# Optimization experiments

Measured on AMD Instinct MI355X. Metric: run time of the kernel, lower is better.

The kernel has to match this reference:

```python
import jax, jax.numpy as jnp
import numpy as np

N = 2048       # num nodes
IN = 512       # in_features == hidden_features == out_features (residuals)
HID = 512
OUT = 512
H = 8          # num_heads
DX = 256       # x feature dim
LN_EPS = 1e-5
NORM_EPS = 1e-12


def _layernorm(x, g, b):
    mu = jnp.mean(x, axis=-1, keepdims=True)
    var = jnp.mean(jnp.square(x - mu), axis=-1, keepdims=True)
    return (x - mu) * jax.lax.rsqrt(var + LN_EPS) * g + b


def _l1_normalize(x):
    # torch F.normalize(p=1): x / max(||x||_1, eps)
    n = jnp.sum(jnp.abs(x), axis=-1, keepdims=True)
    return x / jnp.maximum(n, NORM_EPS)


def _linear_init(key, out_f, in_f):
    kw, kb = jax.random.split(key)
    bound = 1.0 / np.sqrt(in_f)
    W = jax.random.uniform(kw, (out_f, in_f), jnp.float32, -bound, bound)
    b = jax.random.uniform(kb, (out_f,), jnp.float32, -bound, bound)
    return W, b


def setup_inputs() -> dict:
    key = jax.random.key(0)
    ks = jax.random.split(key, 10)
    h = jax.random.normal(ks[0], (N, IN), jnp.float32)
    x = jax.random.uniform(ks[1], (N, DX), jnp.float32)
    Wk, bk = _linear_init(ks[2], HID, IN)
    Wq, bq = _linear_init(ks[3], HID, IN)
    Wv, bv = _linear_init(ks[4], HID, IN)
    Wm1, bm1 = _linear_init(ks[5], H, H + 1)   # mixing_x2h
    Wm2, bm2 = _linear_init(ks[6], 1, H)
    Wfc, bfc = _linear_init(ks[7], OUT, HID + 4)
    ln_g = jnp.ones((IN,), jnp.float32)
    ln_b = jnp.zeros((IN,), jnp.float32)
    lnf_g = jnp.ones((HID,), jnp.float32)
    lnf_b = jnp.zeros((HID,), jnp.float32)
    return dict(h=h, x=x, ln_g=ln_g, ln_b=ln_b, Wk=Wk, bk=bk, Wq=Wq, bq=bq,
                Wv=Wv, bv=bv, Wm1=Wm1, bm1=bm1, Wm2=Wm2, bm2=bm2,
                lnf_g=lnf_g, lnf_b=lnf_b, Wfc=Wfc, bfc=bfc)


def reference(h, x, ln_g, ln_b, Wk, bk, Wq, bq, Wv, bv, Wm1, bm1, Wm2, bm2,
              lnf_g, lnf_b, Wfc, bfc):
    h0, x0 = h, x
    hn = _layernorm(h, ln_g, ln_b)
    xn = _l1_normalize(x)

    k = (hn @ Wk.T + bk).reshape(N, HID // H, H)
    q = (hn @ Wq.T + bq).reshape(N, HID // H, H)
    a_h = jnp.einsum('xyb,zyb->xzb', k, q)          # [N, N, H]
    a_x = xn @ xn.T                                  # [N, N]

    # head mixing: Linear(H+1 -> H) over concat([a_x, a_h])
    a_cat = jnp.concatenate([a_x[..., None], a_h], axis=-1)  # [N, N, H+1]
    a_h = a_cat @ Wm1.T + bm1                                # [N, N, H]
    a_x = (a_h @ Wm2.T + bm2)[..., 0] + a_x                  # [N, N]

    a_h = jax.nn.softmax(a_h, axis=-1)               # softmax over heads
    a_x = _l1_normalize(a_x)

    # per-row stats of a_x -> [N, 4]
    i = jnp.concatenate([
        jnp.diagonal(a_x)[:, None],
        jnp.sum(a_x, axis=-1, keepdims=True),
        jnp.std(a_x, axis=-1, ddof=1, keepdims=True),
        jnp.max(a_x, axis=-1, keepdims=True),
    ], axis=-1)

    v = (hn @ Wv.T + bv).reshape(N, OUT // H, H)
    hm = jnp.einsum('xyb,yzb->xzb', a_h, v).reshape(N, HID)
    xm = a_x @ xn

    hm = hm + h0
    xm = xm + x0
    _h0 = hm

    hf = _layernorm(hm, lnf_g, lnf_b)
    hf = jnp.concatenate([hf, i], axis=-1)           # [N, HID+4]
    hf = jax.nn.elu(hf @ Wfc.T + bfc)
    hf = hf + _h0
    return (hf, xm)
```

## Files before the change

### kernel.cpp

```cpp
#include <hip/hip_runtime.h>
#include <math.h>

#define NN 2048
#define FD 512
#define DXF 256
#define JC 8
#define CHKJ (NN/JC)
#define ITI 32
#define JTW 64
#define NIT (CHKJ/JTW)
#define KC (NN/4)

typedef unsigned short u16;
typedef unsigned int u32;
typedef __attribute__((ext_vector_type(8))) short s16x8;
typedef __attribute__((ext_vector_type(4))) float f32x4;

__device__ __forceinline__ f32x4 MFMA16(s16x8 a, s16x8 b, f32x4 c) {
  return __builtin_amdgcn_mfma_f32_16x16x32_bf16(a, b, c, 0, 0, 0);
}
__device__ __forceinline__ float blo(u32 u) { return __uint_as_float(u << 16); }
__device__ __forceinline__ float bhi(u32 u) { return __uint_as_float(u & 0xffff0000u); }
__device__ __forceinline__ float b2f(u16 v) { return __uint_as_float((u32)v << 16); }
__device__ __forceinline__ u16 bf1(float f) {
  u32 u = __float_as_uint(f);
  u += 0x7fffu + ((u >> 16) & 1u);
  return (u16)(u >> 16);
}
__device__ __forceinline__ u32 pkbf(float a, float b) {
  u32 ua = __float_as_uint(a), ub = __float_as_uint(b);
  ua += 0x7fffu + ((ua >> 16) & 1u);
  ub += 0x7fffu + ((ub >> 16) & 1u);
  return (ua >> 16) | (ub & 0xffff0000u);
}

__global__ void preproc_k(
    const float* __restrict__ h, const float* __restrict__ ln_g,
    const float* __restrict__ ln_b, u16* __restrict__ hnB,
    const float* __restrict__ x, u16* __restrict__ xnB,
    const float* __restrict__ Wk, const float* __restrict__ Wq,
    const float* __restrict__ Wv, u16* __restrict__ wkB, u16* __restrict__ wqB,
    u16* __restrict__ wvB, const float* __restrict__ Wfc, u16* __restrict__ wfcB) {
  int bid = blockIdx.x, t = threadIdx.x;
  __shared__ float red[4][2];
  if (bid < NN) {
    int r = bid;
    float2 v = ((const float2*)(h + (size_t)r * FD))[t];
    float2 w = make_float2(v.x + v.y, v.x * v.x + v.y * v.y);
#pragma unroll
    for (int o = 32; o > 0; o >>= 1) { w.x += __shfl_xor(w.x, o); w.y += __shfl_xor(w.y, o); }
    if ((t & 63) == 0) { red[t >> 6][0] = w.x; red[t >> 6][1] = w.y; }
    __syncthreads();
    float S  = (red[0][0] + red[1][0]) + (red[2][0] + red[3][0]);
    float SQ = (red[0][1] + red[1][1]) + (red[2][1] + red[3][1]);
    float mean = S * (1.f / FD);
    float var  = SQ * (1.f / FD) - mean * mean;
    float rs = rsqrtf(var + 1e-5f);
    float2 gg = ((const float2*)ln_g)[t], bb = ((const float2*)ln_b)[t];
    float ox = (v.x - mean) * rs * gg.x + bb.x;
    float oy = (v.y - mean) * rs * gg.y + bb.y;
    *(u32*)(hnB + (size_t)r * FD + 2 * t) = pkbf(ox, oy);
  } else if (bid < 2 * NN) {
    int r = bid - NN;
    float v = x[(size_t)r * DXF + t];
    float s = fabsf(v);
#pragma unroll
    for (int o = 32; o > 0; o >>= 1) s += __shfl_xor(s, o);
    if ((t & 63) == 0) red[t >> 6][0] = s;
    __syncthreads();
    float S = (red[0][0] + red[1][0]) + (red[2][0] + red[3][0]);
    float inv = 1.f / fmaxf(S, 1e-12f);
    xnB[(size_t)r * DXF + t] = bf1(v * inv);
  } else if (bid < 2 * NN + 1536) {
    int idx = bid - 2 * NN;
    int z = idx >> 9;
    int i = ((idx & 511) << 8) + t;
    const float* W = (z == 0) ? Wk : (z == 1) ? Wq : Wv;
    u16* O = (z == 0) ? wkB : (z == 1) ? wqB : wvB;
    float2 v = ((const float2*)W)[i];
    ((u32*)O)[i] = pkbf(v.x, v.y);
  } else {
    int i = (bid - (2 * NN + 1536)) * 256 + t;
    if (i < 512 * 272) {
      int r = i / 272, c2 = (i - r * 272) * 2;
      float a = (c2 < 516) ? Wfc[r * 516 + c2] : 0.f;
      float b = (c2 + 1 < 516) ? Wfc[r * 516 + c2 + 1] : 0.f;
      ((u32*)wfcB)[i] = pkbf(a, b);
    }
  }
}

__global__ void xnt_k(const u16* __restrict__ xnB, u16* __restrict__ xnTg) {
  __shared__ u16 tile[16][264];
  int t = threadIdx.x;
  int r0 = blockIdx.x * 16;
#pragma unroll
  for (int s = 0; s < 2; ++s) {
    int c = s * 256 + t;
    int db = c & 31, row = c >> 5;
    *(uint4*)&tile[row][db * 8] = *(const uint4*)(xnB + (size_t)(r0 + row) * DXF + db * 8);
  }
  __syncthreads();
#pragma unroll
  for (int s = 0; s < 2; ++s) {
    int c = s * 256 + t;
    int jb = c & 1, d = c >> 1;
    u32 p[4];
#pragma unroll
    for (int e2 = 0; e2 < 4; ++e2) {
      u16 a = tile[jb * 8 + e2 * 2][d], b = tile[jb * 8 + e2 * 2 + 1][d];
      p[e2] = (u32)a | ((u32)b << 16);
    }
    *(uint4*)(xnTg + (size_t)d * NN + r0 + jb * 8) = make_uint4(p[0], p[1], p[2], p[3]);
  }
}

__global__ __launch_bounds__(256) void proj3_k(
    const u16* __restrict__ A,
    const u16* __restrict__ W0, const u16* __restrict__ W1, const u16* __restrict__ W2,
    const float* __restrict__ b0, const float* __restrict__ b1, const float* __restrict__ b2,
    u16* __restrict__ kP, u16* __restrict__ qP, u16* __restrict__ vPT) {
  int z = blockIdx.z;
  const u16* B = (z == 0) ? W0 : (z == 1) ? W1 : W2;
  const float* bias = (z == 0) ? b0 : (z == 1) ? b1 : b2;
  int t = threadIdx.x, w = t >> 6, lane = t & 63, g = lane >> 4, li = lane & 15;
  int m0 = blockIdx.x * 64 + (w & 1) * 32;
  int n0 = blockIdx.y * 64 + (w >> 1) * 32;
  f32x4 acc[2][2] = {};
  for (int k0 = 0; k0 < FD; k0 += 32) {
    s16x8 a0 = *(const s16x8*)(A + (size_t)(m0 + li) * FD + k0 + g * 8);
    s16x8 a1 = *(const s16x8*)(A + (size_t)(m0 + 16 + li) * FD + k0 + g * 8);
    s16x8 bA = *(const s16x8*)(B + (size_t)(n0 + li) * FD + k0 + g * 8);
    s16x8 bB = *(const s16x8*)(B + (size_t)(n0 + 16 + li) * FD + k0 + g * 8);
    acc[0][0] = MFMA16(a0, bA, acc[0][0]);
    acc[0][1] = MFMA16(a0, bB, acc[0][1]);
    acc[1][0] = MFMA16(a1, bA, acc[1][0]);
    acc[1][1] = MFMA16(a1, bB, acc[1][1]);
  }
#pragma unroll
  for (int ms = 0; ms < 2; ++ms)
#pragma unroll
    for (int ns = 0; ns < 2; ++ns) {
      int ncol = n0 + ns * 16 + li;
      float bv = bias[ncol];
      if (z < 2) {
        u16* out = z ? qP : kP;
#pragma unroll
        for (int r = 0; r < 4; ++r) {
          int i = m0 + ms * 16 + g * 4 + r;
          out[((size_t)(ncol & 7) * NN + i) * 64 + (ncol >> 3)] = bf1(acc[ms][ns][r] + bv);
        }
      } else {
        u16 e[4];
#pragma unroll
        for (int r = 0; r < 4; ++r) e[r] = bf1(acc[ms][ns][r] + bv);
        u32 p0 = (u32)e[0] | ((u32)e[1] << 16);
        u32 p1 = (u32)e[2] | ((u32)e[3] << 16);
        int ib = m0 + ms * 16 + g * 4;
        *(uint2*)(vPT + ((size_t)((ncol & 7) * 64 + (ncol >> 3))) * NN + ib) =
            make_uint2(p0, p1);
      }
    }
}

__global__ __launch_bounds__(256) void fc_gemm_k(
    const u16* __restrict__ A, const u16* __restrict__ B,
    const float* __restrict__ bias, const float* __restrict__ res,
    float* __restrict__ C) {
  int t = threadIdx.x, w = t >> 6, lane = t & 63, g = lane >> 4, li = lane & 15;
  int m0 = blockIdx.x * 32 + (w & 1) * 16;
  int n0 = blockIdx.y * 32 + (w >> 1) * 16;
  f32x4 acc = {};
  for (int k0 = 0; k0 < 544; k0 += 32) {
    s16x8 a0 = *(const s16x8*)(A + (size_t)(m0 + li) * 544 + k0 + g * 8);
    s16x8 b0 = *(const s16x8*)(B + (size_t)(n0 + li) * 544 + k0 + g * 8);
    acc = MFMA16(a0, b0, acc);
  }
  int ncol = n0 + li;
  float bv = bias[ncol];
#pragma unroll
  for (int r = 0; r < 4; ++r) {
    int i = m0 + g * 4 + r;
    float cv = acc[r] + bv;
    cv = (cv > 0.f) ? cv : (expf(cv) - 1.f);
    cv += res[(size_t)i * FD + ncol];
    C[(size_t)i * FD + ncol] = cv;
  }
}

__global__ __launch_bounds__(256) void xm_split_k(
    const u16* __restrict__ axg, const u16* __restrict__ xnTg,
    float* __restrict__ xmp, float* __restrict__ stq) {
  int t = threadIdx.x, w = t >> 6, lane = t & 63, g = lane >> 4, li = lane & 15;
  int m0 = blockIdx.x * 64 + (w & 1) * 32;
  int n0 = blockIdx.y * 64 + (w >> 1) * 32;
  int z = blockIdx.z;
  const int kb = z * KC;
  f32x4 acc[2][2] = {};
  float sab[2] = {0.f, 0.f}, ssu[2] = {0.f, 0.f}, ssq[2] = {0.f, 0.f};
  float smx[2] = {-1e30f, -1e30f};
  const bool do_stats = (blockIdx.y == 0) && ((w >> 1) == 0);
  for (int k0 = 0; k0 < KC; k0 += 32) {
    s16x8 a0 = *(const s16x8*)(axg + (size_t)(m0 + li) * NN + kb + k0 + g * 8);
    s16x8 a1 = *(const s16x8*)(axg + (size_t)(m0 + 16 + li) * NN + kb + k0 + g * 8);
    s16x8 bA = *(const s16x8*)(xnTg + (size_t)(n0 + li) * NN + kb + k0 + g * 8);
    s16x8 bB = *(const s16x8*)(xnTg + (size_t)(n0 + 16 + li) * NN + kb + k0 + g * 8);
    acc[0][0] = MFMA16(a0, bA, acc[0][0]);
    acc[0][1] = MFMA16(a0, bB, acc[0][1]);
    acc[1][0] = MFMA16(a1, bA, acc[1][0]);
    acc[1][1] = MFMA16(a1, bB, acc[1][1]);
    if (do_stats) {
#pragma unroll
      for (int ms = 0; ms < 2; ++ms) {
        u32 pu[4];
        *(s16x8*)pu = ms ? a1 : a0;
#pragma unroll
        for (int q2 = 0; q2 < 4; ++q2) {
          float x0 = blo(pu[q2]), x1 = bhi(pu[q2]);
          sab[ms] += fabsf(x0) + fabsf(x1);
          ssu[ms] += x0 + x1;
          ssq[ms] += x0 * x0 + x1 * x1;
          smx[ms] = fmaxf(smx[ms], fmaxf(x0, x1));
        }
      }
    }
  }
  if (do_stats) {
#pragma unroll
    for (int off = 16; off < 64; off <<= 1) {
#pragma unroll
      for (int ms = 0; ms < 2; ++ms) {
        sab[ms] += __shfl_xor(sab[ms], off);
        ssu[ms] += __shfl_xor(ssu[ms], off);
        ssq[ms] += __shfl_xor(ssq[ms], off);
        smx[ms] = fmaxf(smx[ms], __shfl_xor(smx[ms], off));
      }
    }
    if (g == 0) {
#pragma unroll
      for (int ms = 0; ms < 2; ++ms) {
        size_t base = ((size_t)z * NN + m0 + ms * 16 + li) * 4;
        stq[base + 0] = sab[ms]; stq[base + 1] = ssu[ms];
        stq[base + 2] = ssq[ms]; stq[base + 3] = smx[ms];
      }
    }
  }
#pragma unroll
  for (int ms = 0; ms < 2; ++ms)
#pragma unroll
    for (int ns = 0; ns < 2; ++ns) {
      int ncol = n0 + ns * 16 + li;
#pragma unroll
      for (int r = 0; r < 4; ++r) {
        int i = m0 + ms * 16 + g * 4 + r;
        xmp[(size_t)z * NN * DXF + (size_t)i * DXF + ncol] = acc[ms][ns][r];
      }
    }
}

__global__ __launch_bounds__(512, 2) void fused_mfma_k(
    const u16* __restrict__ kP, const u16* __restrict__ qP,
    const u16* __restrict__ vPT, const u16* __restrict__ xnB,
    const float* __restrict__ Wm1, const float* __restrict__ bm1,
    const float* __restrict__ Wm2, const float* __restrict__ bm2,
    u16* __restrict__ hmPart, u16* __restrict__ axg, float* __restrict__ stPd) {
  __shared__ __align__(16) unsigned char L[81920];
  const int O_KI = 0, O_XNI = 32768, O_P = 49152;
  const int t = threadIdx.x, w = t >> 6, lane = t & 63;
  const int g = lane >> 4, li = lane & 15;
  const int i0 = blockIdx.x * ITI, chunk = blockIdx.y;
  const int si = w & 1;
  const int jL = (w >> 1) * 16 + li;
  const int iRow = si * 16 + li;
  const int prow = si * 16 + li;

  float W1[8][9], B1v[8], w2v[8];
#pragma unroll
  for (int o = 0; o < 8; ++o) {
    B1v[o] = bm1[o];
    w2v[o] = Wm2[o];
#pragma unroll
    for (int b3 = 0; b3 < 9; ++b3) W1[o][b3] = Wm1[o * 9 + b3];
  }
  const float b2v = bm2[0];

#pragma unroll
  for (int s = 0; s < 4; ++s) {
    int c = s * 512 + t;
    int yb = c & 7, il = (c >> 3) & 31, b = c >> 8;
    uint4 v = *(const uint4*)(kP + ((size_t)b * NN + i0 + il) * 64 + yb * 8);
    *(uint4*)(L + O_KI + b * 4096 + il * 128 + ((yb ^ (il & 7)) << 4)) = v;
  }
#pragma unroll
  for (int s = 0; s < 2; ++s) {
    int c = s * 512 + t;
    int db = c & 31, il = c >> 5;
    uint4 v = *(const uint4*)(xnB + (size_t)(i0 + il) * DXF + db * 8);
    *(uint4*)(L + O_XNI + il * 512 + ((db ^ (il & 7)) << 4)) = v;
  }
  __syncthreads();

  f32x4 hmA[2][4];
#pragma unroll
  for (int a = 0; a < 2; ++a)
#pragma unroll
    for (int c = 0; c < 4; ++c) hmA[a][c] = (f32x4)(0.f);

  for (int it = 0; it < NIT; ++it) {
    const int j0 = chunk * CHKJ + it * JTW;
    f32x4 accS[9];
#pragma unroll
    for (int a = 0; a < 9; ++a) accS[a] = (f32x4)(0.f);
#pragma unroll
    for (int b = 0; b < 8; ++b)
#pragma unroll
      for (int ks = 0; ks < 2; ++ks) {
        int blk = ks * 4 + g;
        s16x8 af = *(const s16x8*)(L + O_KI + b * 4096 + iRow * 128 +
                                   ((blk ^ (iRow & 7)) << 4));
        s16x8 bf = *(const s16x8*)(qP + ((size_t)b * NN + j0 + jL) * 64 + ks * 32 + g * 8);
        accS[b] = MFMA16(af, bf, accS[b]);
      }
#pragma unroll
    for (int ks = 0; ks < 8; ++ks) {
      int blk = ks * 4 + g;
      s16x8 af = *(const s16x8*)(L + O_XNI + iRow * 512 + ((blk ^ (iRow & 7)) << 4));
      s16x8 bf = *(const s16x8*)(xnB + (size_t)(j0 + jL) * DXF + ks * 32 + g * 8);
      accS[8] = MFMA16(af, bf, accS[8]);
    }
    s16x8 vf0[2][4];
#pragma unroll
    for (int kb = 0; kb < 2; ++kb)
#pragma unroll
      for (int zt = 0; zt < 4; ++zt)
        vf0[kb][zt] = *(const s16x8*)(vPT + ((size_t)((w >> 1) * 2 + 0) * 64 + zt * 16 + li) * NN +
                                      j0 + kb * 32 + g * 8);
    __syncthreads();
#pragma unroll
    for (int r = 0; r < 4; ++r) {
      float sb[8];
#pragma unroll
      for (int b = 0; b < 8; ++b) sb[b] = accS[b][r];
      float ax = accS[8][r];
      float m[8];
#pragma unroll
      for (int o = 0; o < 8; ++o) {
        float a = B1v[o] + W1[o][0] * ax;
#pragma unroll
        for (int b = 0; b < 8; ++b) a += W1[o][1 + b] * sb[b];
        m[o] = a;
      }
      float axn = b2v + ax;
#pragma unroll
      for (int o = 0; o < 8; ++o) axn += w2v[o] * m[o];
      const int iL2 = si * 16 + g * 4 + r;
      const int iG = i0 + iL2, jG = j0 + jL;
      axg[(size_t)iG * NN + jG] = bf1(axn);
      if (iG == jG) stPd[iG] = axn;
      float mx = m[0];
#pragma unroll
      for (int o = 1; o < 8; ++o) mx = fmaxf(mx, m[o]);
      float es[8], esum = 0.f;
#pragma unroll
      for (int o = 0; o < 8; ++o) { es[o] = __expf(m[o] - mx); esum += es[o]; }
      float inv = 1.f / esum;
      const int base = iL2 * 128 + (((jL >> 3) ^ (iL2 & 7)) << 4) + (jL & 7) * 2;
#pragma unroll
      for (int b = 0; b < 8; ++b)
        *(u16*)(L + O_P + b * 4096 + base) = bf1(es[b] * inv);
    }
    s16x8 vf1[2][4];
#pragma unroll
    for (int kb = 0; kb < 2; ++kb)
#pragma unroll
      for (int zt = 0; zt < 4; ++zt)
        vf1[kb][zt] = *(const s16x8*)(vPT + ((size_t)((w >> 1) * 2 + 1) * 64 + zt * 16 + li) * NN +
                                      j0 + kb * 32 + g * 8);
    __syncthreads();
#pragma unroll
    for (int hh = 0; hh < 2; ++hh) {
      const int hd = (w >> 1) * 2 + hh;
#pragma unroll
      for (int kb = 0; kb < 2; ++kb) {
        s16x8 pa = *(const s16x8*)(L + O_P + hd * 4096 + prow * 128 +
                                   (((kb * 4 + g) ^ (prow & 7)) << 4));
#pragma unroll
        for (int zt = 0; zt < 4; ++zt) {
          s16x8 vf = hh ? vf1[kb][zt] : vf0[kb][zt];
          hmA[hh][zt] = MFMA16(pa, vf, hmA[hh][zt]);
        }
      }
    }
  }
#pragma unroll
  for (int hh = 0; hh < 2; ++hh) {
    const int hd = (w >> 1) * 2 + hh;
#pragma unroll
    for (int zt = 0; zt < 4; ++zt)
#pragma unroll
      for (int r = 0; r < 4; ++r) {
        int i = i0 + si * 16 + g * 4 + r;
        int z = zt * 16 + li;
        hmPart[((size_t)(chunk * 8 + hd) * NN + i) * 64 + z] = bf1(hmA[hh][zt][r]);
      }
  }
}

__global__ void epilogue1_k(
    const float* __restrict__ h, const float* __restrict__ x,
    const u16* __restrict__ hmp, const float* __restrict__ xmp,
    const float* __restrict__ stq, const float* __restrict__ stPd,
    const float* __restrict__ lnf_g, const float* __restrict__ lnf_b,
    float* __restrict__ hmf, u16* __restrict__ hfeB, float* __restrict__ out_xm) {
  int r = blockIdx.x, t = threadIdx.x;
  int c0 = 2 * t, c1 = c0 + 1;
  float2 acc = ((const float2*)(h + (size_t)r * FD))[t];
#pragma unroll
  for (int ch = 0; ch < JC; ++ch) {
    acc.x += b2f(hmp[((size_t)(ch * 8 + (c0 & 7)) * NN + r) * 64 + (c0 >> 3)]);
    acc.y += b2f(hmp[((size_t)(ch * 8 + (c1 & 7)) * NN + r) * 64 + (c1 >> 3)]);
  }
  ((float2*)(hmf + (size_t)r * FD))[t] = acc;
  float2 w = make_float2(acc.x + acc.y, acc.x * acc.x + acc.y * acc.y);
#pragma unroll
  for (int o = 32; o > 0; o >>= 1) { w.x += __shfl_xor(w.x, o); w.y += __shfl_xor(w.y, o); }
  __shared__ float red[4][2];
  __shared__ float s_inv;
  if ((t & 63) == 0) { red[t >> 6][0] = w.x; red[t >> 6][1] = w.y; }
  __syncthreads();
  float S  = (red[0][0] + red[1][0]) + (red[2][0] + red[3][0]);
  float SQ = (red[0][1] + red[1][1]) + (red[2][1] + red[3][1]);
  float mean = S * (1.f / FD);
  float var  = SQ * (1.f / FD) - mean * mean;
  float rs = rsqrtf(var + 1e-5f);
  float2 g2 = ((const float2*)lnf_g)[t], b2 = ((const float2*)lnf_b)[t];
  float ox = (acc.x - mean) * rs * g2.x + b2.x;
  float oy = (acc.y - mean) * rs * g2.y + b2.y;
  *(u32*)(hfeB + (size_t)r * 544 + c0) = pkbf(ox, oy);
  if (t == 0) {
    float sab = 0.f, ssu = 0.f, ssq = 0.f, smx = -1e30f;
#pragma unroll
    for (int c = 0; c < 4; ++c) {
      size_t b = ((size_t)c * NN + r) * 4;
      sab += stq[b + 0]; ssu += stq[b + 1]; ssq += stq[b + 2];
      smx = fmaxf(smx, stq[b + 3]);
    }
    float diag = stPd[r];
    float L1 = fmaxf(sab, 1e-12f);
    float inv = 1.f / L1;
    float stdv = sqrtf(fmaxf((ssq - ssu * ssu * (1.f / 2048.f)) * (1.f / 2047.f), 0.f)) * inv;
    u16* he = hfeB + (size_t)r * 544;
    he[512] = bf1(diag * inv); he[513] = bf1(ssu * inv);
    he[514] = bf1(stdv);       he[515] = bf1(smx * inv);
    s_inv = inv;
  }
  if (t < 14) *(u32*)(hfeB + (size_t)r * 544 + 516 + 2 * t) = 0;
  __syncthreads();
  float inv = s_inv;
  float xv = xmp[(size_t)r * DXF + t] + xmp[(size_t)NN * DXF + (size_t)r * DXF + t] +
             xmp[2 * (size_t)NN * DXF + (size_t)r * DXF + t] +
             xmp[3 * (size_t)NN * DXF + (size_t)r * DXF + t];
  out_xm[(size_t)r * DXF + t] = xv * inv + x[(size_t)r * DXF + t];
}

extern "C" void kernel_launch(void* const* d_in, const int* in_sizes, int n_in,
                              void* d_out, int out_size, void* d_ws, size_t ws_size,
                              hipStream_t stream) {
  (void)in_sizes; (void)n_in; (void)out_size; (void)ws_size;
  const float* h    = (const float*)d_in[0];
  const float* x    = (const float*)d_in[1];
  const float* ln_g = (const float*)d_in[2];
  const float* ln_b = (const float*)d_in[3];
  const float* Wk   = (const float*)d_in[4];
  const float* bk   = (const float*)d_in[5];
  const float* Wq   = (const float*)d_in[6];
  const float* bq   = (const float*)d_in[7];
  const float* Wv   = (const float*)d_in[8];
  const float* bv   = (const float*)d_in[9];
  const float* Wm1  = (const float*)d_in[10];
  const float* bm1  = (const float*)d_in[11];
  const float* Wm2  = (const float*)d_in[12];
  const float* bm2  = (const float*)d_in[13];
  const float* lnf_g = (const float*)d_in[14];
  const float* lnf_b = (const float*)d_in[15];
  const float* Wfc  = (const float*)d_in[16];
  const float* bfc  = (const float*)d_in[17];

  char* wsb = (char*)d_ws;
  size_t off = 0;
  auto alloc = [&](size_t bytes) { char* p = wsb + off; off += (bytes + 255) & ~(size_t)255; return p; };
  u16*   hnB  = (u16*)alloc((size_t)NN * FD * 2);
  u16*   wkB  = (u16*)alloc((size_t)FD * FD * 2);
  u16*   wqB  = (u16*)alloc((size_t)FD * FD * 2);
  u16*   wvB  = (u16*)alloc((size_t)FD * FD * 2);
  u16*   wfcB = (u16*)alloc((size_t)512 * 544 * 2);
  u16*   kP   = (u16*)alloc((size_t)8 * NN * 64 * 2);
  u16*   qP   = (u16*)alloc((size_t)8 * NN * 64 * 2);
  u16*   vPT  = (u16*)alloc((size_t)8 * 64 * NN * 2);
  u16*   xnB  = (u16*)alloc((size_t)NN * DXF * 2);
  u16*   xnTg = (u16*)alloc((size_t)DXF * NN * 2);
  u16*   axg  = (u16*)alloc((size_t)NN * NN * 2);
  u16*   hmp  = (u16*)alloc((size_t)JC * 8 * NN * 64 * 2);
  float* xmp  = (float*)alloc((size_t)4 * NN * DXF * 4);
  float* stq  = (float*)alloc((size_t)4 * NN * 4 * 4);
  float* stPd = (float*)alloc((size_t)NN * 4);
  float* hmf  = (float*)alloc((size_t)NN * FD * 4);
  u16*   hfeB = (u16*)alloc((size_t)NN * 544 * 2);
  float* out_hf = (float*)d_out;
  float* out_xm = out_hf + (size_t)NN * FD;

  preproc_k<<<2 * NN + 1536 + 544, 256, 0, stream>>>(
      h, ln_g, ln_b, hnB, x, xnB, Wk, Wq, Wv, wkB, wqB, wvB, Wfc, wfcB);
  xnt_k<<<NN / 16, 256, 0, stream>>>(xnB, xnTg);

  proj3_k<<<dim3(32, 8, 3), 256, 0, stream>>>(hnB, wkB, wqB, wvB, bk, bq, bv, kP, qP, vPT);

  fused_mfma_k<<<dim3(NN / ITI, JC), 512, 0, stream>>>(kP, qP, vPT, xnB, Wm1, bm1, Wm2, bm2,
                                                       hmp, axg, stPd);

  xm_split_k<<<dim3(32, 4, 4), 256, 0, stream>>>(axg, xnTg, xmp, stq);

  epilogue1_k<<<NN, 256, 0, stream>>>(h, x, hmp, xmp, stq, stPd, lnf_g, lnf_b, hmf, hfeB, out_xm);

  fc_gemm_k<<<dim3(64, 16), 256, 0, stream>>>(hfeB, wfcB, bfc, hmf, out_hf);
}
```

Baseline: 159.7 us.

## Store q, v and xn in MFMA-fragment order for contiguous wave loads

The projection kernel now writes q and v, and the transpose kernel writes a copy of xn, pre-arranged in per-lane MFMA operand order. The fused attention kernel can then load each B fragment as one contiguous 1 KB block per wave instead of strided rows. This targets uncoalesced global loads in the main loop. In exchange the producer kernels use more complex scattered stores, and the extra xn copy adds some memory traffic.

New measurement: 141.7 us, median of 2. 11.3% less time.

```diff
diff --git a/kernel.cpp b/kernel.cpp
--- a/kernel.cpp
+++ b/kernel.cpp
@@ -90,7 +90,8 @@
   }
 }
 
-__global__ void xnt_k(const u16* __restrict__ xnB, u16* __restrict__ xnTg) {
+__global__ void xnt_k(const u16* __restrict__ xnB, u16* __restrict__ xnTg,
+                      u16* __restrict__ xnF) {
   __shared__ u16 tile[16][264];
   int t = threadIdx.x;
   int r0 = blockIdx.x * 16;
@@ -113,13 +114,21 @@
     }
     *(uint4*)(xnTg + (size_t)d * NN + r0 + jb * 8) = make_uint4(p[0], p[1], p[2], p[3]);
   }
+#pragma unroll
+  for (int s = 0; s < 2; ++s) {
+    int idx = s * 256 + t;
+    int ks = idx >> 6, lane = idx & 63;
+    int row = lane & 15, db = ks * 32 + (lane >> 4) * 8;
+    uint4 v = *(const uint4*)&tile[row][db];
+    *(uint4*)(xnF + (((size_t)(r0 >> 4) * 8 + ks) * 64 + lane) * 8) = v;
+  }
 }
 
 __global__ __launch_bounds__(256) void proj3_k(
     const u16* __restrict__ A,
     const u16* __restrict__ W0, const u16* __restrict__ W1, const u16* __restrict__ W2,
     const float* __restrict__ b0, const float* __restrict__ b1, const float* __restrict__ b2,
-    u16* __restrict__ kP, u16* __restrict__ qP, u16* __restrict__ vPT) {
+    u16* __restrict__ kP, u16* __restrict__ qF, u16* __restrict__ vF) {
   int z = blockIdx.z;
   const u16* B = (z == 0) ? W0 : (z == 1) ? W1 : W2;
   const float* bias = (z == 0) ? b0 : (z == 1) ? b1 : b2;
@@ -143,22 +152,33 @@
     for (int ns = 0; ns < 2; ++ns) {
       int ncol = n0 + ns * 16 + li;
       float bv = bias[ncol];
-      if (z < 2) {
-        u16* out = z ? qP : kP;
+      if (z == 0) {
 #pragma unroll
         for (int r = 0; r < 4; ++r) {
           int i = m0 + ms * 16 + g * 4 + r;
-          out[((size_t)(ncol & 7) * NN + i) * 64 + (ncol >> 3)] = bf1(acc[ms][ns][r] + bv);
+          kP[((size_t)(ncol & 7) * NN + i) * 64 + (ncol >> 3)] = bf1(acc[ms][ns][r] + bv);
+        }
+      } else if (z == 1) {
+#pragma unroll
+        for (int r = 0; r < 4; ++r) {
+          int i = m0 + ms * 16 + g * 4 + r;
+          size_t idx = ((size_t)(i >> 4) * 8 + (ncol & 7)) * 1024 +
+                       (size_t)(ncol >> 8) * 512 +
+                       (size_t)((i & 15) | (((ncol >> 6) & 3) << 4)) * 8 +
+                       ((ncol >> 3) & 7);
+          qF[idx] = bf1(acc[ms][ns][r] + bv);
         }
       } else {
-        u16 e[4];
-#pragma unroll
-        for (int r = 0; r < 4; ++r) e[r] = bf1(acc[ms][ns][r] + bv);
-        u32 p0 = (u32)e[0] | ((u32)e[1] << 16);
-        u32 p1 = (u32)e[2] | ((u32)e[3] << 16);
-        int ib = m0 + ms * 16 + g * 4;
-        *(uint2*)(vPT + ((size_t)((ncol & 7) * 64 + (ncol >> 3))) * NN + ib) =
-            make_uint2(p0, p1);
+        u16 e4[4];
+#pragma unroll
+        for (int r = 0; r < 4; ++r) e4[r] = bf1(acc[ms][ns][r] + bv);
+        u32 p0 = (u32)e4[0] | ((u32)e4[1] << 16);
+        u32 p1 = (u32)e4[2] | ((u32)e4[3] << 16);
+        int ibase = m0 + ms * 16 + g * 4;
+        int lane_w = ((ncol >> 3) & 15) | (((ibase >> 3) & 3) << 4);
+        size_t base = ((((size_t)(m0 >> 5) * 8 + (ncol & 7)) * 4 + (ncol >> 7)) * 64 + lane_w) * 8 +
+                      ((g & 1) * 4);
+        *(uint2*)(vF + base) = make_uint2(p0, p1);
       }
     }
 }
@@ -259,8 +279,9 @@
 }
 
 __global__ __launch_bounds__(512, 2) void fused_mfma_k(
-    const u16* __restrict__ kP, const u16* __restrict__ qP,
-    const u16* __restrict__ vPT, const u16* __restrict__ xnB,
+    const u16* __restrict__ kP, const u16* __restrict__ qF,
+    const u16* __restrict__ vF, const u16* __restrict__ xnB,
+    const u16* __restrict__ xnF,
     const float* __restrict__ Wm1, const float* __restrict__ bm1,
     const float* __restrict__ Wm2, const float* __restrict__ bm2,
     u16* __restrict__ hmPart, u16* __restrict__ axg, float* __restrict__ stPd) {
@@ -270,7 +291,8 @@
   const int g = lane >> 4, li = lane & 15;
   const int i0 = blockIdx.x * ITI, chunk = blockIdx.y;
   const int si = w & 1;
-  const int jL = (w >> 1) * 16 + li;
+  const int jw = w >> 1;
+  const int jL = jw * 16 + li;
   const int iRow = si * 16 + li;
   const int prow = si * 16 + li;
 
@@ -308,6 +330,8 @@
 
   for (int it = 0; it < NIT; ++it) {
     const int j0 = chunk * CHKJ + it * JTW;
+    const int jt = (j0 >> 4) + jw;
+    const int jb32 = j0 >> 5;
     f32x4 accS[9];
 #pragma unroll
     for (int a = 0; a < 9; ++a) accS[a] = (f32x4)(0.f);
@@ -318,14 +342,15 @@
         int blk = ks * 4 + g;
         s16x8 af = *(const s16x8*)(L + O_KI + b * 4096 + iRow * 128 +
                                    ((blk ^ (iRow & 7)) << 4));
-        s16x8 bf = *(const s16x8*)(qP + ((size_t)b * NN + j0 + jL) * 64 + ks * 32 + g * 8);
+        s16x8 bf = *(const s16x8*)(qF + (((size_t)jt * 8 + b) * 2 + ks) * 512 +
+                                   (size_t)lane * 8);
         accS[b] = MFMA16(af, bf, accS[b]);
       }
 #pragma unroll
     for (int ks = 0; ks < 8; ++ks) {
       int blk = ks * 4 + g;
       s16x8 af = *(const s16x8*)(L + O_XNI + iRow * 512 + ((blk ^ (iRow & 7)) << 4));
-      s16x8 bf = *(const s16x8*)(xnB + (size_t)(j0 + jL) * DXF + ks * 32 + g * 8);
+      s16x8 bf = *(const s16x8*)(xnF + ((size_t)jt * 8 + ks) * 512 + (size_t)lane * 8);
       accS[8] = MFMA16(af, bf, accS[8]);
     }
     s16x8 vf0[2][4];
@@ -333,8 +358,8 @@
     for (int kb = 0; kb < 2; ++kb)
 #pragma unroll
       for (int zt = 0; zt < 4; ++zt)
-        vf0[kb][zt] = *(const s16x8*)(vPT + ((size_t)((w >> 1) * 2 + 0) * 64 + zt * 16 + li) * NN +
-                                      j0 + kb * 32 + g * 8);
+        vf0[kb][zt] = *(const s16x8*)(vF + ((((size_t)(jb32 + kb) * 8 + jw * 2 + 0) * 4 + zt) * 512) +
+                                      (size_t)lane * 8);
     __syncthreads();
 #pragma unroll
     for (int r = 0; r < 4; ++r) {
@@ -374,12 +399,12 @@
     for (int kb = 0; kb < 2; ++kb)
 #pragma unroll
       for (int zt = 0; zt < 4; ++zt)
-        vf1[kb][zt] = *(const s16x8*)(vPT + ((size_t)((w >> 1) * 2 + 1) * 64 + zt * 16 + li) * NN +
-                                      j0 + kb * 32 + g * 8);
+        vf1[kb][zt] = *(const s16x8*)(vF + ((((size_t)(jb32 + kb) * 8 + jw * 2 + 1) * 4 + zt) * 512) +
+                                      (size_t)lane * 8);
     __syncthreads();
 #pragma unroll
     for (int hh = 0; hh < 2; ++hh) {
-      const int hd = (w >> 1) * 2 + hh;
+      const int hd = jw * 2 + hh;
 #pragma unroll
       for (int kb = 0; kb < 2; ++kb) {
         s16x8 pa = *(const s16x8*)(L + O_P + hd * 4096 + prow * 128 +
@@ -394,7 +419,7 @@
   }
 #pragma unroll
   for (int hh = 0; hh < 2; ++hh) {
-    const int hd = (w >> 1) * 2 + hh;
+    const int hd = jw * 2 + hh;
 #pragma unroll
     for (int zt = 0; zt < 4; ++zt)
 #pragma unroll
@@ -495,10 +520,11 @@
   u16*   wvB  = (u16*)alloc((size_t)FD * FD * 2);
   u16*   wfcB = (u16*)alloc((size_t)512 * 544 * 2);
   u16*   kP   = (u16*)alloc((size_t)8 * NN * 64 * 2);
-  u16*   qP   = (u16*)alloc((size_t)8 * NN * 64 * 2);
-  u16*   vPT  = (u16*)alloc((size_t)8 * 64 * NN * 2);
+  u16*   qF   = (u16*)alloc((size_t)8 * NN * 64 * 2);
+  u16*   vF   = (u16*)alloc((size_t)8 * 64 * NN * 2);
   u16*   xnB  = (u16*)alloc((size_t)NN * DXF * 2);
   u16*   xnTg = (u16*)alloc((size_t)DXF * NN * 2);
+  u16*   xnF  = (u16*)alloc((size_t)NN * DXF * 2);
   u16*   axg  = (u16*)alloc((size_t)NN * NN * 2);
   u16*   hmp  = (u16*)alloc((size_t)JC * 8 * NN * 64 * 2);
   float* xmp  = (float*)alloc((size_t)4 * NN * DXF * 4);
@@ -511,11 +537,12 @@
 
   preproc_k<<<2 * NN + 1536 + 544, 256, 0, stream>>>(
       h, ln_g, ln_b, hnB, x, xnB, Wk, Wq, Wv, wkB, wqB, wvB, Wfc, wfcB);
-  xnt_k<<<NN / 16, 256, 0, stream>>>(xnB, xnTg);
-
-  proj3_k<<<dim3(32, 8, 3), 256, 0, stream>>>(hnB, wkB, wqB, wvB, bk, bq, bv, kP, qP, vPT);
-
-  fused_mfma_k<<<dim3(NN / ITI, JC), 512, 0, stream>>>(kP, qP, vPT, xnB, Wm1, bm1, Wm2, bm2,
+  xnt_k<<<NN / 16, 256, 0, stream>>>(xnB, xnTg, xnF);
+
+  proj3_k<<<dim3(32, 8, 3), 256, 0, stream>>>(hnB, wkB, wqB, wvB, bk, bq, bv, kP, qF, vF);
+
+  fused_mfma_k<<<dim3(NN / ITI, JC), 512, 0, stream>>>(kP, qF, vF, xnB, xnF,
+                                                       Wm1, bm1, Wm2, bm2,
                                                        hmp, axg, stPd);
 
   xm_split_k<<<dim3(32, 4, 4), 256, 0, stream>>>(axg, xnTg, xmp, stq);
```

## Store k, q, xn in MFMA fragment order and drop LDS staging

Applied to the files above, without the earlier changes.

The projection kernel now writes k and q, and the transpose kernel writes xn, directly in 16x16x32 MFMA fragment order. Each lane then loads its operand with one contiguous 16-byte global read. Because of this, the fused attention kernel no longer stages the i-side k and xn tiles in shared memory, and its LDS footprint shrinks from 80 KB to 32 KB, which could allow more resident blocks. In exchange, the i-side operands are reread from global or cache on every j iteration instead of once from LDS, and the scattered 2-byte stores in the projection kernel take a different access pattern.

Measured after the change: 149.2 us. -6.6%, faster.

```diff
diff --git a/kernel.cpp b/kernel.cpp
--- a/kernel.cpp
+++ b/kernel.cpp
@@ -90,7 +90,8 @@
   }
 }
 
-__global__ void xnt_k(const u16* __restrict__ xnB, u16* __restrict__ xnTg) {
+__global__ void xnt_k(const u16* __restrict__ xnB, u16* __restrict__ xnTg,
+                      u16* __restrict__ xnF) {
   __shared__ u16 tile[16][264];
   int t = threadIdx.x;
   int r0 = blockIdx.x * 16;
@@ -113,13 +114,21 @@
     }
     *(uint4*)(xnTg + (size_t)d * NN + r0 + jb * 8) = make_uint4(p[0], p[1], p[2], p[3]);
   }
+#pragma unroll
+  for (int s = 0; s < 2; ++s) {
+    int idx = s * 256 + t;
+    int ks = idx >> 6, lane = idx & 63;
+    int row = lane & 15, db = ks * 32 + (lane >> 4) * 8;
+    uint4 v = *(const uint4*)&tile[row][db];
+    *(uint4*)(xnF + (((size_t)(r0 >> 4) * 8 + ks) * 64 + lane) * 8) = v;
+  }
 }
 
 __global__ __launch_bounds__(256) void proj3_k(
     const u16* __restrict__ A,
     const u16* __restrict__ W0, const u16* __restrict__ W1, const u16* __restrict__ W2,
     const float* __restrict__ b0, const float* __restrict__ b1, const float* __restrict__ b2,
-    u16* __restrict__ kP, u16* __restrict__ qP, u16* __restrict__ vPT) {
+    u16* __restrict__ kF, u16* __restrict__ qF, u16* __restrict__ vPT) {
   int z = blockIdx.z;
   const u16* B = (z == 0) ? W0 : (z == 1) ? W1 : W2;
   const float* bias = (z == 0) ? b0 : (z == 1) ? b1 : b2;
@@ -144,11 +153,15 @@
       int ncol = n0 + ns * 16 + li;
       float bv = bias[ncol];
       if (z < 2) {
-        u16* out = z ? qP : kP;
+        u16* out = z ? qF : kF;
 #pragma unroll
         for (int r = 0; r < 4; ++r) {
           int i = m0 + ms * 16 + g * 4 + r;
-          out[((size_t)(ncol & 7) * NN + i) * 64 + (ncol >> 3)] = bf1(acc[ms][ns][r] + bv);
+          size_t idx = ((size_t)(i >> 4) * 8 + (ncol & 7)) * 1024 +
+                       (size_t)(ncol >> 8) * 512 +
+                       (size_t)((i & 15) | (((ncol >> 6) & 3) << 4)) * 8 +
+                       ((ncol >> 3) & 7);
+          out[idx] = bf1(acc[ms][ns][r] + bv);
         }
       } else {
         u16 e[4];
@@ -259,20 +272,20 @@
 }
 
 __global__ __launch_bounds__(512, 2) void fused_mfma_k(
-    const u16* __restrict__ kP, const u16* __restrict__ qP,
-    const u16* __restrict__ vPT, const u16* __restrict__ xnB,
+    const u16* __restrict__ kF, const u16* __restrict__ qF,
+    const u16* __restrict__ vPT, const u16* __restrict__ xnF,
     const float* __restrict__ Wm1, const float* __restrict__ bm1,
     const float* __restrict__ Wm2, const float* __restrict__ bm2,
     u16* __restrict__ hmPart, u16* __restrict__ axg, float* __restrict__ stPd) {
-  __shared__ __align__(16) unsigned char L[81920];
-  const int O_KI = 0, O_XNI = 32768, O_P = 49152;
+  __shared__ __align__(16) unsigned char L[32768];
   const int t = threadIdx.x, w = t >> 6, lane = t & 63;
   const int g = lane >> 4, li = lane & 15;
   const int i0 = blockIdx.x * ITI, chunk = blockIdx.y;
   const int si = w & 1;
-  const int jL = (w >> 1) * 16 + li;
-  const int iRow = si * 16 + li;
+  const int jw = w >> 1;
+  const int jL = jw * 16 + li;
   const int prow = si * 16 + li;
+  const int itile = (i0 >> 4) + si;
 
   float W1[8][9], B1v[8], w2v[8];
 #pragma unroll
@@ -284,22 +297,6 @@
   }
   const float b2v = bm2[0];
 
-#pragma unroll
-  for (int s = 0; s < 4; ++s) {
-    int c = s * 512 + t;
-    int yb = c & 7, il = (c >> 3) & 31, b = c >> 8;
-    uint4 v = *(const uint4*)(kP + ((size_t)b * NN + i0 + il) * 64 + yb * 8);
-    *(uint4*)(L + O_KI + b * 4096 + il * 128 + ((yb ^ (il & 7)) << 4)) = v;
-  }
-#pragma unroll
-  for (int s = 0; s < 2; ++s) {
-    int c = s * 512 + t;
-    int db = c & 31, il = c >> 5;
-    uint4 v = *(const uint4*)(xnB + (size_t)(i0 + il) * DXF + db * 8);
-    *(uint4*)(L + O_XNI + il * 512 + ((db ^ (il & 7)) << 4)) = v;
-  }
-  __syncthreads();
-
   f32x4 hmA[2][4];
 #pragma unroll
   for (int a = 0; a < 2; ++a)
@@ -308,6 +305,7 @@
 
   for (int it = 0; it < NIT; ++it) {
     const int j0 = chunk * CHKJ + it * JTW;
+    const int jt = (j0 >> 4) + jw;
     f32x4 accS[9];
 #pragma unroll
     for (int a = 0; a < 9; ++a) accS[a] = (f32x4)(0.f);
@@ -315,17 +313,16 @@
     for (int b = 0; b < 8; ++b)
 #pragma unroll
       for (int ks = 0; ks < 2; ++ks) {
-        int blk = ks * 4 + g;
-        s16x8 af = *(const s16x8*)(L + O_KI + b * 4096 + iRow * 128 +
-                                   ((blk ^ (iRow & 7)) << 4));
-        s16x8 bf = *(const s16x8*)(qP + ((size_t)b * NN + j0 + jL) * 64 + ks * 32 + g * 8);
+        s16x8 af = *(const s16x8*)(kF + (((size_t)itile * 8 + b) * 2 + ks) * 512 +
+                                   (size_t)lane * 8);
+        s16x8 bf = *(const s16x8*)(qF + (((size_t)jt * 8 + b) * 2 + ks) * 512 +
+                                   (size_t)lane * 8);
         accS[b] = MFMA16(af, bf, accS[b]);
       }
 #pragma unroll
     for (int ks = 0; ks < 8; ++ks) {
-      int blk = ks * 4 + g;
-      s16x8 af = *(const s16x8*)(L + O_XNI + iRow * 512 + ((blk ^ (iRow & 7)) << 4));
-      s16x8 bf = *(const s16x8*)(xnB + (size_t)(j0 + jL) * DXF + ks * 32 + g * 8);
+      s16x8 af = *(const s16x8*)(xnF + ((size_t)itile * 8 + ks) * 512 + (size_t)lane * 8);
+      s16x8 bf = *(const s16x8*)(xnF + ((size_t)jt * 8 + ks) * 512 + (size_t)lane * 8);
       accS[8] = MFMA16(af, bf, accS[8]);
     }
     s16x8 vf0[2][4];
@@ -333,7 +330,8 @@
     for (int kb = 0; kb < 2; ++kb)
 #pragma unroll
       for (int zt = 0; zt < 4; ++zt)
-        vf0[kb][zt] = *(const s16x8*)(vPT + ((size_t)((w >> 1) * 2 + 0) * 64 + zt * 16 + li) * NN +
+        vf0[kb][zt] = *(const s16x8*)(vPT + ((size_t)(jw * 2 + 0) * 64 * NN +
+                                      (size_t)(zt * 16 + li) * NN) +
                                       j0 + kb * 32 + g * 8);
     __syncthreads();
 #pragma unroll
@@ -367,22 +365,23 @@
       const int base = iL2 * 128 + (((jL >> 3) ^ (iL2 & 7)) << 4) + (jL & 7) * 2;
 #pragma unroll
       for (int b = 0; b < 8; ++b)
-        *(u16*)(L + O_P + b * 4096 + base) = bf1(es[b] * inv);
+        *(u16*)(L + b * 4096 + base) = bf1(es[b] * inv);
     }
     s16x8 vf1[2][4];
 #pragma unroll
     for (int kb = 0; kb < 2; ++kb)
 #pragma unroll
       for (int zt = 0; zt < 4; ++zt)
-        vf1[kb][zt] = *(const s16x8*)(vPT + ((size_t)((w >> 1) * 2 + 1) * 64 + zt * 16 + li) * NN +
+        vf1[kb][zt] = *(const s16x8*)(vPT + ((size_t)(jw * 2 + 1) * 64 * NN +
+                                      (size_t)(zt * 16 + li) * NN) +
                                       j0 + kb * 32 + g * 8);
     __syncthreads();
 #pragma unroll
     for (int hh = 0; hh < 2; ++hh) {
-      const int hd = (w >> 1) * 2 + hh;
+      const int hd = jw * 2 + hh;
 #pragma unroll
       for (int kb = 0; kb < 2; ++kb) {
-        s16x8 pa = *(const s16x8*)(L + O_P + hd * 4096 + prow * 128 +
+        s16x8 pa = *(const s16x8*)(L + hd * 4096 + prow * 128 +
                                    (((kb * 4 + g) ^ (prow & 7)) << 4));
 #pragma unroll
         for (int zt = 0; zt < 4; ++zt) {
@@ -394,7 +393,7 @@
   }
 #pragma unroll
   for (int hh = 0; hh < 2; ++hh) {
-    const int hd = (w >> 1) * 2 + hh;
+    const int hd = jw * 2 + hh;
 #pragma unroll
     for (int zt = 0; zt < 4; ++zt)
 #pragma unroll
@@ -494,11 +493,12 @@
   u16*   wqB  = (u16*)alloc((size_t)FD * FD * 2);
   u16*   wvB  = (u16*)alloc((size_t)FD * FD * 2);
   u16*   wfcB = (u16*)alloc((size_t)512 * 544 * 2);
-  u16*   kP   = (u16*)alloc((size_t)8 * NN * 64 * 2);
-  u16*   qP   = (u16*)alloc((size_t)8 * NN * 64 * 2);
+  u16*   kF   = (u16*)alloc((size_t)8 * NN * 64 * 2);
+  u16*   qF   = (u16*)alloc((size_t)8 * NN * 64 * 2);
   u16*   vPT  = (u16*)alloc((size_t)8 * 64 * NN * 2);
   u16*   xnB  = (u16*)alloc((size_t)NN * DXF * 2);
   u16*   xnTg = (u16*)alloc((size_t)DXF * NN * 2);
+  u16*   xnF  = (u16*)alloc((size_t)NN * DXF * 2);
   u16*   axg  = (u16*)alloc((size_t)NN * NN * 2);
   u16*   hmp  = (u16*)alloc((size_t)JC * 8 * NN * 64 * 2);
   float* xmp  = (float*)alloc((size_t)4 * NN * DXF * 4);
@@ -511,11 +511,12 @@
 
   preproc_k<<<2 * NN + 1536 + 544, 256, 0, stream>>>(
       h, ln_g, ln_b, hnB, x, xnB, Wk, Wq, Wv, wkB, wqB, wvB, Wfc, wfcB);
-  xnt_k<<<NN / 16, 256, 0, stream>>>(xnB, xnTg);
-
-  proj3_k<<<dim3(32, 8, 3), 256, 0, stream>>>(hnB, wkB, wqB, wvB, bk, bq, bv, kP, qP, vPT);
-
-  fused_mfma_k<<<dim3(NN / ITI, JC), 512, 0, stream>>>(kP, qP, vPT, xnB, Wm1, bm1, Wm2, bm2,
+  xnt_k<<<NN / 16, 256, 0, stream>>>(xnB, xnTg, xnF);
+
+  proj3_k<<<dim3(32, 8, 3), 256, 0, stream>>>(hnB, wkB, wqB, wvB, bk, bq, bv, kF, qF, vPT);
+
+  fused_mfma_k<<<dim3(NN / ITI, JC), 512, 0, stream>>>(kF, qF, vPT, xnF,
+                                                       Wm1, bm1, Wm2, bm2,
                                                        hmp, axg, stPd);
 
   xm_split_k<<<dim3(32, 4, 4), 256, 0, stream>>>(axg, xnTg, xmp, stq);
```
